# Kernel optimization log

Hardware: AMD Instinct MI355X
Metric: run time of the kernel (lower is better)

## Reference

```python
import jax, jax.numpy as jnp
import numpy as np

NINF = -1000000000.0
B, S, E = 2, 4096, 1024


def setup_inputs() -> dict:
    key = jax.random.key(0)
    ks = jax.random.split(key, 10)
    scale = 1.0 / np.sqrt(E)
    return {
        "query": jax.random.normal(ks[0], (B, S, E), dtype=jnp.float32),
        "key": jax.random.normal(ks[1], (B, S, E), dtype=jnp.float32),
        "value": jax.random.normal(ks[2], (B, S, E), dtype=jnp.float32),
        "mask": jax.random.randint(ks[3], (S, S), 0, 2).astype(bool),
        "Wq": jax.random.normal(ks[4], (E, E), dtype=jnp.float32) * scale,
        "bq": jnp.zeros((E,), dtype=jnp.float32),
        "Wk": jax.random.normal(ks[5], (E, E), dtype=jnp.float32) * scale,
        "bk": jnp.zeros((E,), dtype=jnp.float32),
        "Wv": jax.random.normal(ks[6], (E, E), dtype=jnp.float32) * scale,
        "bv": jnp.zeros((E,), dtype=jnp.float32),
    }


def reference(query, key, value, mask, Wq, bq, Wk, bk, Wv, bv):
    # linear projections (nn.Linear convention: x @ W.T + b)
    q = jnp.einsum('bse,fe->bsf', query, Wq) + bq   # [B,S,E]
    k = jnp.einsum('bse,fe->bsf', key, Wk) + bk
    v = jnp.einsum('bse,fe->bsf', value, Wv) + bv
    # full QK^T score matrix [B,S,S], scaled by sqrt(E) of projected query
    scores = jnp.einsum('bqe,bke->bqk', q, k) / jnp.sqrt(jnp.float32(E))
    scores = jnp.where(mask, jnp.float32(NINF), scores)  # True = ignored
    attn = jax.nn.softmax(scores, axis=-1)
    return jnp.einsum('bqk,bkv->bqv', attn, v)
```

## Files before the change

### kernel.cpp

```cpp
#include <hip/hip_runtime.h>
#include <hip/hip_bf16.h>


typedef _Float16 f16_t;
typedef _Float16 f16x8 __attribute__((ext_vector_type(8)));
typedef float f32x4 __attribute__((ext_vector_type(4)));
typedef unsigned long long u64;
typedef unsigned int uint;

union PackH8 { f16x8 v; f16_t e[8]; };

__device__ __forceinline__ f32x4 mfma_f16(f16x8 a, f16x8 b, f32x4 c) {
  return __builtin_amdgcn_mfma_f32_16x16x32_f16(a, b, c, 0, 0, 0);
}

__device__ __forceinline__ void cp16(const f16_t* g, f16_t* l) {
  __builtin_amdgcn_global_load_lds(
      (const __attribute__((address_space(1))) unsigned int*)g,
      (__attribute__((address_space(3))) unsigned int*)l, 16, 0, 0);
}

__global__ __launch_bounds__(256) void cvt_mask(
    const float* __restrict__ q, const float* __restrict__ k,
    const float* __restrict__ v, const float* __restrict__ wq,
    const float* __restrict__ wk, const float* __restrict__ wv,
    const int* __restrict__ mask,
    f16_t* __restrict__ xq, f16_t* __restrict__ xk, f16_t* __restrict__ xv,
    f16_t* __restrict__ wqh, f16_t* __restrict__ wkh, f16_t* __restrict__ wvh,
    u64* __restrict__ mb) {
  if (blockIdx.y == 6) {
    const int lane = threadIdx.x & 63;
    int wid = blockIdx.x * 4 + (threadIdx.x >> 6);
    for (int w = wid; w < 262144; w += 16384) {
      const int pred = mask[(size_t)w * 64 + lane] != 0;
      u64 b = __ballot(pred);
      if (lane == 0) mb[w] = b;
    }
    return;
  }
  const float* src; f16_t* dst; size_t n;
  switch (blockIdx.y) {
    case 0: src = q;  dst = xq;  n = 8388608; break;
    case 1: src = k;  dst = xk;  n = 8388608; break;
    case 2: src = v;  dst = xv;  n = 8388608; break;
    case 3: src = wq; dst = wqh; n = 1048576; break;
    case 4: src = wk; dst = wkh; n = 1048576; break;
    default: src = wv; dst = wvh; n = 1048576; break;
  }
  size_t i = ((size_t)blockIdx.x * 256 + threadIdx.x) * 8;
  if (i >= n) return;
  float4 a = *(const float4*)(src + i);
  float4 b = *(const float4*)(src + i + 4);
  PackH8 p;
  p.e[0] = (f16_t)a.x; p.e[1] = (f16_t)a.y; p.e[2] = (f16_t)a.z; p.e[3] = (f16_t)a.w;
  p.e[4] = (f16_t)b.x; p.e[5] = (f16_t)b.y; p.e[6] = (f16_t)b.z; p.e[7] = (f16_t)b.w;
  *(f16x8*)(dst + i) = p.v;
}

#define TK 64

__device__ __forceinline__ void core8ph(
    const f16_t* __restrict__ Ab, const f16_t* __restrict__ Bb,
    int m0, int n0, int K, int iters, f32x4 (&acc)[4][8]) {
  __shared__ f16_t lA[32768];
  __shared__ f16_t lB[32768];

  const int tid = threadIdx.x;
  const int w = tid >> 6, lane = tid & 63;
  const int quad = lane >> 4, l15 = lane & 15;
  const int wm = w >> 1, wn = w & 1;
  const int srow = lane >> 2;
  const int sg = (lane & 3) ^ (srow & 3);
  const int Km = K - 1;

  const uint aoff0 = (uint)(m0 + w * 32 + srow) * K + sg * 8;
  const uint aoff1 = aoff0 + 16 * K;
  const uint boff0 = (uint)(n0 + w * 32 + srow) * K + sg * 8;
  const uint boff1 = boff0 + 16 * K;
  const int ld0 = (w * 32) * 32;
  const int ld1 = (w * 32 + 16) * 32;

  int afo[4], bfo[8];
  const int swz = (quad ^ (l15 & 3)) * 8;
#pragma unroll
  for (int mi = 0; mi < 4; mi++) afo[mi] = (wm * 64 + mi * 16 + l15) * 32 + swz;
#pragma unroll
  for (int ni = 0; ni < 8; ni++) bfo[ni] = (wn * 128 + ni * 16 + l15) * 32 + swz;

#define STG_A(sl, kb) { cp16(Ab + aoff0 + (kb), lA + (sl) * 8192 + ld0); \
                        cp16(Ab + aoff1 + (kb), lA + (sl) * 8192 + ld1); }
#define STG_B(sl, kb) { cp16(Bb + boff0 + (kb), lB + (sl) * 8192 + ld0); \
                        cp16(Bb + boff1 + (kb), lB + (sl) * 8192 + ld1); }

  STG_A(0, 0) STG_B(0, 0)
  STG_A(1, 32) STG_B(1, 32)
  STG_A(2, 64) STG_B(2, 64)
  asm volatile("s_waitcnt vmcnt(4)" ::: "memory");
  __builtin_amdgcn_s_barrier();

  f16x8 af[4], bf[8];

#define PH(SL, Q, STG, VMW) { \
    if ((Q) == 0) { \
      _Pragma("unroll") for (int mi = 0; mi < 4; mi++) \
        af[mi] = *(const f16x8*)(lA + (SL) * 8192 + afo[mi]); \
      _Pragma("unroll") for (int ni = 0; ni < 4; ni++) \
        bf[ni] = *(const f16x8*)(lB + (SL) * 8192 + bfo[ni]); \
    } else { \
      _Pragma("unroll") for (int ni = 4; ni < 8; ni++) \
        bf[ni] = *(const f16x8*)(lB + (SL) * 8192 + bfo[ni]); \
    } \
    STG \
    asm volatile("" ::: "memory"); \
    __builtin_amdgcn_s_barrier(); \
    asm volatile("s_waitcnt lgkmcnt(0)" ::: "memory"); \
    __builtin_amdgcn_sched_barrier(0); \
    __builtin_amdgcn_s_setprio(1); \
    _Pragma("unroll") for (int mi = 0; mi < 4; mi++) { \
      _Pragma("unroll") for (int nj = 0; nj < 4; nj++) { \
        const int ni = (Q) * 4 + nj; \
        acc[mi][ni] = mfma_f16(af[mi], bf[ni], acc[mi][ni]); \
      } } \
    __builtin_amdgcn_sched_barrier(0); \
    __builtin_amdgcn_s_setprio(0); \
    VMW \
    asm volatile("" ::: "memory"); \
    __builtin_amdgcn_s_barrier(); \
  }

#define VM4 asm volatile("s_waitcnt vmcnt(4)" ::: "memory");

  for (int i = 0; i < iters; i++) {
    const int t0 = 2 * i;
    const int kb3 = ((t0 + 1) * 64 + 32) & Km;
    const int kb0 = ((t0 + 2) * 64) & Km;
    const int kb1 = kb0 + 32;
    const int kb2 = ((t0 + 3) * 64) & Km;
    PH(0, 0, STG_A(3, kb3), )
    PH(0, 1, STG_B(3, kb3), )
    PH(1, 0, STG_A(0, kb0), )
    PH(1, 1, STG_B(0, kb0), VM4)
    PH(2, 0, STG_A(1, kb1), )
    PH(2, 1, STG_B(1, kb1), )
    PH(3, 0, STG_A(2, kb2), )
    PH(3, 1, STG_B(2, kb2), VM4)
  }

  asm volatile("s_waitcnt vmcnt(0)" ::: "memory");
#undef PH
#undef VM4
#undef STG_A
#undef STG_B
}

__global__ __launch_bounds__(512, 2) void gemm512(
    const f16_t* __restrict__ A, const f16_t* __restrict__ B,
    f16_t* __restrict__ C, const float* __restrict__ bias0,
    const float* __restrict__ bias1, int K,
    long sAz, long sBz, long sCz, float scale0, float scale1, int Cstride) {
  const int bz = blockIdx.z;
  const int n0 = blockIdx.x * 256;
  const int m0 = blockIdx.y * 256;
  const f16_t* Ab = A + (size_t)sAz * bz;
  const f16_t* Bb = B + (size_t)sBz * bz;

  f32x4 acc[4][8] = {};
  core8ph(Ab, Bb, m0, n0, K, K >> 7, acc);

  const int tid = threadIdx.x;
  const int w = tid >> 6, lane = tid & 63;
  const int quad = lane >> 4, l15 = lane & 15;
  const int wm = w >> 1, wn = w & 1;
  const float* bias = bz ? bias1 : bias0;
  const float scale = bz ? scale1 : scale0;
  f16_t* Cb = C + (size_t)sCz * bz;
#pragma unroll
  for (int mi = 0; mi < 4; mi++) {
#pragma unroll
    for (int ni = 0; ni < 8; ni++) {
      const int gm0 = m0 + wm * 64 + mi * 16 + quad * 4;
      const int gn = n0 + wn * 128 + ni * 16 + l15;
#pragma unroll
      for (int r = 0; r < 4; r++) {
        const int gm = gm0 + r;
        Cb[(size_t)gm * Cstride + gn] = (f16_t)((acc[mi][ni][r] + bias[gn]) * scale);
      }
    }
  }
}

__global__ __launch_bounds__(256, 2) void gemm256(
    const f16_t* __restrict__ A, const f16_t* __restrict__ B,
    f16_t* __restrict__ C, const float* __restrict__ bias0, int K) {
  __shared__ f16_t sA[256 * TK];
  __shared__ f16_t sB[128 * TK];

  const int n0 = blockIdx.x * 128;
  const int m0 = blockIdx.y * 256;
  const int tid = threadIdx.x;
  const int w = tid >> 6, lane = tid & 63;
  const int quad = lane >> 4, l15 = lane & 15;
  const int lr = lane >> 3, ls = lane & 7;
  const int sw = ls ^ lr;

  const f16_t* ga[8];
  const f16_t* gb[4];
#pragma unroll
  for (int j = 0; j < 8; j++)
    ga[j] = A + (size_t)(m0 + w * 64 + j * 8 + lr) * K + sw * 8;
#pragma unroll
  for (int j = 0; j < 4; j++)
    gb[j] = B + (size_t)(n0 + w * 32 + j * 8 + lr) * K + sw * 8;

  f32x4 acc[4][8] = {};

  for (int k0 = 0; k0 < K; k0 += TK) {
    __syncthreads();
#pragma unroll
    for (int j = 0; j < 8; j++) cp16(ga[j] + k0, &sA[(w * 64 + j * 8) * TK]);
#pragma unroll
    for (int j = 0; j < 4; j++) cp16(gb[j] + k0, &sB[(w * 32 + j * 8) * TK]);
    __syncthreads();
#pragma unroll
    for (int ks = 0; ks < 2; ks++) {
      f16x8 af[4], bf[8];
#pragma unroll
      for (int mi = 0; mi < 4; mi++) {
        const int row = w * 64 + mi * 16 + l15;
        const int sg = (ks * 4 + quad) ^ (row & 7);
        af[mi] = *(const f16x8*)&sA[row * TK + sg * 8];
      }
#pragma unroll
      for (int ni = 0; ni < 8; ni++) {
        const int row = ni * 16 + l15;
        const int sg = (ks * 4 + quad) ^ (row & 7);
        bf[ni] = *(const f16x8*)&sB[row * TK + sg * 8];
      }
#pragma unroll
      for (int mi = 0; mi < 4; mi++)
#pragma unroll
        for (int ni = 0; ni < 8; ni++)
          acc[mi][ni] = mfma_f16(af[mi], bf[ni], acc[mi][ni]);
    }
  }

#pragma unroll
  for (int mi = 0; mi < 4; mi++) {
#pragma unroll
    for (int ni = 0; ni < 8; ni++) {
      const int gm0 = m0 + w * 64 + mi * 16 + quad * 4;
      const int gn = n0 + ni * 16 + l15;
#pragma unroll
      for (int r = 0; r < 4; r++) {
        const int gm = gm0 + r;
        const int bb = gn >> 12;
        const int s = gn & 4095;
        C[(size_t)bb * 4194304 + (size_t)gm * 4096 + s] =
            (f16_t)(acc[mi][ni][r] + bias0[gm]);
      }
    }
  }
}

__global__ __launch_bounds__(512, 2) void gemm_qk(
    const f16_t* __restrict__ A, const f16_t* __restrict__ B,
    f16_t* __restrict__ S, const u64* __restrict__ mb,
    float* __restrict__ lrow) {
  const int bz = blockIdx.z;
  const int n0 = blockIdx.x * 256;
  const int m0 = blockIdx.y * 256;
  const f16_t* Ab = A + (size_t)4194304 * bz;
  const f16_t* Bb = B + (size_t)4194304 * bz;

  f32x4 acc[4][8] = {};
  core8ph(Ab, Bb, m0, n0, 1024, 8, acc);

  const int tid = threadIdx.x;
  const int w = tid >> 6, lane = tid & 63;
  const int quad = lane >> 4, l15 = lane & 15;
  const int wm = w >> 1, wn = w & 1;
  f16_t* Sb = S + (size_t)16777216 * bz;
  float* lb = lrow + bz * 4096;
  const int wbase = (n0 >> 6) + wn * 2;
#pragma unroll
  for (int mi = 0; mi < 4; mi++) {
#pragma unroll
    for (int r = 0; r < 4; r++) {
      const int gm = m0 + wm * 64 + mi * 16 + quad * 4 + r;
      const u64 w0 = mb[(size_t)gm * 64 + wbase];
      const u64 w1 = mb[(size_t)gm * 64 + wbase + 1];
      float rs = 0.f;
#pragma unroll
      for (int ni = 0; ni < 8; ni++) {
        const int col_l = ni * 16 + l15;
        const u64 mw = (ni < 4) ? w0 : w1;
        const int bit = (int)((mw >> (col_l & 63)) & 1);
        const float p = bit ? 0.f : __expf(acc[mi][ni][r] - 3.0f);
        Sb[(size_t)gm * 4096 + n0 + wn * 128 + col_l] = (f16_t)p;
        rs += p;
      }
      rs += __shfl_xor(rs, 1); rs += __shfl_xor(rs, 2);
      rs += __shfl_xor(rs, 4); rs += __shfl_xor(rs, 8);
      if (l15 == 0) atomicAdd(&lb[gm], rs);
    }
  }
}

__global__ __launch_bounds__(256) void gemm_pv(
    const f16_t* __restrict__ S, const f16_t* __restrict__ V,
    float* __restrict__ O, const float* __restrict__ lrow) {
  __shared__ f16_t sA[128 * TK];
  __shared__ f16_t sB[128 * TK];
  const int bid = blockIdx.x;
  const int bz = bid >> 8;
  const int r8 = bid & 255;
  const int xcd = r8 & 7;
  const int j = r8 >> 3;
  const int m0 = (xcd * 4 + (j >> 3)) * 128;
  const int n0 = (j & 7) * 128;

  const int tid = threadIdx.x;
  const int w = tid >> 6, lane = tid & 63;
  const int quad = lane >> 4, l15 = lane & 15;
  const int wm = w >> 1, wn = w & 1;
  const int lr = lane >> 3, ls = lane & 7;
  const int sw = ls ^ lr;

  const f16_t* Ab = S + (size_t)16777216 * bz;
  const f16_t* Bb = V + (size_t)4194304 * bz;

  const f16_t* ga[4];
  const f16_t* gb[4];
#pragma unroll
  for (int jj = 0; jj < 4; jj++) {
    ga[jj] = Ab + (size_t)(m0 + w * 32 + jj * 8 + lr) * 4096 + sw * 8;
    gb[jj] = Bb + (size_t)(n0 + w * 32 + jj * 8 + lr) * 4096 + sw * 8;
  }

  f32x4 acc[4][4] = {};

  for (int k0 = 0; k0 < 4096; k0 += TK) {
    __syncthreads();
#pragma unroll
    for (int jj = 0; jj < 4; jj++) {
      cp16(ga[jj] + k0, &sA[(w * 32 + jj * 8) * TK]);
      cp16(gb[jj] + k0, &sB[(w * 32 + jj * 8) * TK]);
    }
    __syncthreads();
#pragma unroll
    for (int ks = 0; ks < 2; ks++) {
      f16x8 af[4], bf[4];
#pragma unroll
      for (int mi = 0; mi < 4; mi++) {
        const int row = wm * 64 + mi * 16 + l15;
        const int sg = (ks * 4 + quad) ^ (row & 7);
        af[mi] = *(const f16x8*)&sA[row * TK + sg * 8];
      }
#pragma unroll
      for (int ni = 0; ni < 4; ni++) {
        const int row = wn * 64 + ni * 16 + l15;
        const int sg = (ks * 4 + quad) ^ (row & 7);
        bf[ni] = *(const f16x8*)&sB[row * TK + sg * 8];
      }
#pragma unroll
      for (int mi = 0; mi < 4; mi++)
#pragma unroll
        for (int ni = 0; ni < 4; ni++)
          acc[mi][ni] = mfma_f16(af[mi], bf[ni], acc[mi][ni]);
    }
  }

  float* Ob = O + (size_t)4194304 * bz;
  const float* lb = lrow + bz * 4096;
#pragma unroll
  for (int mi = 0; mi < 4; mi++) {
#pragma unroll
    for (int ni = 0; ni < 4; ni++) {
      const int gm0 = m0 + wm * 64 + mi * 16 + quad * 4;
      const int gn = n0 + wn * 64 + ni * 16 + l15;
#pragma unroll
      for (int r = 0; r < 4; r++) {
        const int gm = gm0 + r;
        Ob[(size_t)gm * 1024 + gn] = acc[mi][ni][r] * (1.0f / lb[gm]);
      }
    }
  }
}

extern "C" void kernel_launch(void* const* d_in, const int* in_sizes, int n_in,
                              void* d_out, int out_size, void* d_ws, size_t ws_size,
                              hipStream_t stream) {
  const float* query = (const float*)d_in[0];
  const float* key_  = (const float*)d_in[1];
  const float* value = (const float*)d_in[2];
  const int* mask    = (const int*)d_in[3];
  const float* Wq = (const float*)d_in[4];
  const float* bq = (const float*)d_in[5];
  const float* Wk = (const float*)d_in[6];
  const float* bk = (const float*)d_in[7];
  const float* Wv = (const float*)d_in[8];
  const float* bv = (const float*)d_in[9];
  float* out = (float*)d_out;

  const size_t MB = (size_t)1 << 20;
  char* w = (char*)d_ws;
  f16_t* qb  = (f16_t*)(w);
  f16_t* kb  = (f16_t*)(w + 16 * MB);
  f16_t* vt  = (f16_t*)(w + 32 * MB);
  f16_t* xq  = (f16_t*)(w + 48 * MB);
  f16_t* xk  = (f16_t*)(w + 64 * MB);
  f16_t* xv  = (f16_t*)(w + 80 * MB);
  f16_t* wqh = (f16_t*)(w + 96 * MB);
  f16_t* wkh = (f16_t*)(w + 98 * MB);
  f16_t* wvh = (f16_t*)(w + 100 * MB);
  f16_t* S   = (f16_t*)(w + 48 * MB);
  float* ls  = (float*)(w + 112 * MB);
  u64* mb = (u64*)d_out;

  cvt_mask<<<dim3(4096, 7), 256, 0, stream>>>(query, key_, value, Wq, Wk, Wv,
                                              mask, xq, xk, xv, wqh, wkh, wvh, mb);
  gemm512<<<dim3(4, 32, 2), 512, 0, stream>>>(
      xq, wqh, qb, bq, bk, 1024, 8388608L, 1048576L, 8388608L,
      0.03125f, 1.0f, 1024);
  gemm256<<<dim3(64, 4), 256, 0, stream>>>(wvh, xv, vt, bv, 1024);
  hipMemsetAsync(ls, 0, 2 * 4096 * sizeof(float), stream);
  gemm_qk<<<dim3(16, 16, 2), 512, 0, stream>>>(qb, kb, S, mb, ls);
  gemm_pv<<<dim3(512), 256, 0, stream>>>(S, vt, out, ls);
}
```

Measured before the change: 433.5 us.

## Port V-projection and PV GEMMs to multi-stage pipelined core, remap QK blocks per XCD

Adds a 4-stage pipelined 256x128 GEMM core (core4ph) with async global-to-LDS loads and phase barriers, and uses it for the V projection and the PV GEMM in place of their single-buffered loops. The PV GEMM moves from 128x128 tiles on 256 threads to 256x128 tiles on 512 threads, and the QK GEMM gets a flat grid with XCD-aware block remapping for L2 locality. The main loop now peels its last iteration, so no wrapped-around prefetches are issued and the K mask is dropped. The LDS swizzle pattern is also changed. This adds complexity and raises LDS use per block.

```diff
diff --git a/kernel.cpp b/kernel.cpp
--- a/kernel.cpp
+++ b/kernel.cpp
@@ -70,8 +70,7 @@
   const int quad = lane >> 4, l15 = lane & 15;
   const int wm = w >> 1, wn = w & 1;
   const int srow = lane >> 2;
-  const int sg = (lane & 3) ^ (srow & 3);
-  const int Km = K - 1;
+  const int sg = (lane & 3) ^ ((lane >> 3) & 3);
 
   const uint aoff0 = (uint)(m0 + w * 32 + srow) * K + sg * 8;
   const uint aoff1 = aoff0 + 16 * K;
@@ -81,7 +80,7 @@
   const int ld1 = (w * 32 + 16) * 32;
 
   int afo[4], bfo[8];
-  const int swz = (quad ^ (l15 & 3)) * 8;
+  const int swz = (quad ^ ((l15 >> 1) & 3)) * 8;
 #pragma unroll
   for (int mi = 0; mi < 4; mi++) afo[mi] = (wm * 64 + mi * 16 + l15) * 32 + swz;
 #pragma unroll
@@ -129,13 +128,14 @@
   }
 
 #define VM4 asm volatile("s_waitcnt vmcnt(4)" ::: "memory");
-
-  for (int i = 0; i < iters; i++) {
+#define VM0 asm volatile("s_waitcnt vmcnt(0)" ::: "memory");
+
+  for (int i = 0; i < iters - 1; i++) {
     const int t0 = 2 * i;
-    const int kb3 = ((t0 + 1) * 64 + 32) & Km;
-    const int kb0 = ((t0 + 2) * 64) & Km;
+    const int kb3 = (t0 + 1) * 64 + 32;
+    const int kb0 = (t0 + 2) * 64;
     const int kb1 = kb0 + 32;
-    const int kb2 = ((t0 + 3) * 64) & Km;
+    const int kb2 = (t0 + 3) * 64;
     PH(0, 0, STG_A(3, kb3), )
     PH(0, 1, STG_B(3, kb3), )
     PH(1, 0, STG_A(0, kb0), )
@@ -145,12 +145,103 @@
     PH(3, 0, STG_A(2, kb2), )
     PH(3, 1, STG_B(2, kb2), VM4)
   }
-
-  asm volatile("s_waitcnt vmcnt(0)" ::: "memory");
+  {
+    const int kbp = K - 32;
+    PH(0, 0, STG_A(3, kbp), )
+    PH(0, 1, STG_B(3, kbp), )
+    PH(1, 0, , )
+    PH(1, 1, , VM0)
+    PH(2, 0, , )
+    PH(2, 1, , )
+    PH(3, 0, , )
+    PH(3, 1, , )
+  }
 #undef PH
-#undef VM4
 #undef STG_A
 #undef STG_B
+}
+
+__device__ __forceinline__ void core4ph(
+    const f16_t* __restrict__ Ab, const f16_t* __restrict__ Bb,
+    int m0, int n0, int K, int iters, f32x4 (&acc)[4][4]) {
+  __shared__ f16_t lA[32768];
+  __shared__ f16_t lB[16384];
+
+  const int tid = threadIdx.x;
+  const int w = tid >> 6, lane = tid & 63;
+  const int quad = lane >> 4, l15 = lane & 15;
+  const int wm = w >> 1, wn = w & 1;
+  const int sg = (lane & 3) ^ ((lane >> 3) & 3);
+
+  const uint arow = (uint)(w * 16 + (lane >> 2));
+  const uint aoff0 = (uint)(m0 + arow) * K + sg * 8;
+  const uint aoff1 = aoff0 + 128 * K;
+  const uint boff  = (uint)(n0 + arow) * K + sg * 8;
+  const int ldw = w * 512;
+
+  int afo[4], bfo[4];
+  const int swz = (quad ^ ((l15 >> 1) & 3)) * 8;
+#pragma unroll
+  for (int mi = 0; mi < 4; mi++) afo[mi] = (wm * 64 + mi * 16 + l15) * 32 + swz;
+#pragma unroll
+  for (int ni = 0; ni < 4; ni++) bfo[ni] = (wn * 64 + ni * 16 + l15) * 32 + swz;
+
+#define STG4(sl, kb) { cp16(Ab + aoff0 + (kb), lA + (sl) * 8192 + ldw); \
+                       cp16(Ab + aoff1 + (kb), lA + (sl) * 8192 + 4096 + ldw); \
+                       cp16(Bb + boff  + (kb), lB + (sl) * 4096 + ldw); }
+
+  STG4(0, 0)
+  STG4(1, 32)
+  STG4(2, 64)
+  asm volatile("s_waitcnt vmcnt(3)" ::: "memory");
+  __builtin_amdgcn_s_barrier();
+
+  f16x8 af[4], bf[4];
+
+#define PH4(SL, STG, VMW) { \
+    _Pragma("unroll") for (int mi = 0; mi < 4; mi++) \
+      af[mi] = *(const f16x8*)(lA + (SL) * 8192 + afo[mi]); \
+    _Pragma("unroll") for (int ni = 0; ni < 4; ni++) \
+      bf[ni] = *(const f16x8*)(lB + (SL) * 4096 + bfo[ni]); \
+    STG \
+    asm volatile("" ::: "memory"); \
+    __builtin_amdgcn_s_barrier(); \
+    asm volatile("s_waitcnt lgkmcnt(0)" ::: "memory"); \
+    __builtin_amdgcn_sched_barrier(0); \
+    __builtin_amdgcn_s_setprio(1); \
+    _Pragma("unroll") for (int mi = 0; mi < 4; mi++) { \
+      _Pragma("unroll") for (int ni = 0; ni < 4; ni++) { \
+        acc[mi][ni] = mfma_f16(af[mi], bf[ni], acc[mi][ni]); \
+      } } \
+    __builtin_amdgcn_sched_barrier(0); \
+    __builtin_amdgcn_s_setprio(0); \
+    VMW \
+    asm volatile("" ::: "memory"); \
+    __builtin_amdgcn_s_barrier(); \
+  }
+
+#define VM6 asm volatile("s_waitcnt vmcnt(6)" ::: "memory");
+#define VM3 asm volatile("s_waitcnt vmcnt(3)" ::: "memory");
+
+  for (int i = 0; i < iters - 1; i++) {
+    const int t0 = 2 * i;
+    PH4(0, STG4(3, (t0 + 1) * 64 + 32), VM6)
+    PH4(1, STG4(0, (t0 + 2) * 64), VM6)
+    PH4(2, STG4(1, (t0 + 2) * 64 + 32), VM6)
+    PH4(3, STG4(2, (t0 + 3) * 64), VM6)
+  }
+  {
+    PH4(0, STG4(3, K - 32), VM6)
+    PH4(1, , VM3)
+    PH4(2, , VM0)
+    PH4(3, , )
+  }
+#undef PH4
+#undef STG4
+#undef VM6
+#undef VM3
+#undef VM4
+#undef VM0
 }
 
 __global__ __launch_bounds__(512, 2) void gemm512(
@@ -189,67 +280,25 @@
   }
 }
 
-__global__ __launch_bounds__(256, 2) void gemm256(
+__global__ __launch_bounds__(512, 2) void gemm256(
     const f16_t* __restrict__ A, const f16_t* __restrict__ B,
     f16_t* __restrict__ C, const float* __restrict__ bias0, int K) {
-  __shared__ f16_t sA[256 * TK];
-  __shared__ f16_t sB[128 * TK];
-
   const int n0 = blockIdx.x * 128;
   const int m0 = blockIdx.y * 256;
-  const int tid = threadIdx.x;
-  const int w = tid >> 6, lane = tid & 63;
-  const int quad = lane >> 4, l15 = lane & 15;
-  const int lr = lane >> 3, ls = lane & 7;
-  const int sw = ls ^ lr;
-
-  const f16_t* ga[8];
-  const f16_t* gb[4];
-#pragma unroll
-  for (int j = 0; j < 8; j++)
-    ga[j] = A + (size_t)(m0 + w * 64 + j * 8 + lr) * K + sw * 8;
-#pragma unroll
-  for (int j = 0; j < 4; j++)
-    gb[j] = B + (size_t)(n0 + w * 32 + j * 8 + lr) * K + sw * 8;
-
-  f32x4 acc[4][8] = {};
-
-  for (int k0 = 0; k0 < K; k0 += TK) {
-    __syncthreads();
-#pragma unroll
-    for (int j = 0; j < 8; j++) cp16(ga[j] + k0, &sA[(w * 64 + j * 8) * TK]);
-#pragma unroll
-    for (int j = 0; j < 4; j++) cp16(gb[j] + k0, &sB[(w * 32 + j * 8) * TK]);
-    __syncthreads();
-#pragma unroll
-    for (int ks = 0; ks < 2; ks++) {
-      f16x8 af[4], bf[8];
-#pragma unroll
-      for (int mi = 0; mi < 4; mi++) {
-        const int row = w * 64 + mi * 16 + l15;
-        const int sg = (ks * 4 + quad) ^ (row & 7);
-        af[mi] = *(const f16x8*)&sA[row * TK + sg * 8];
-      }
-#pragma unroll
-      for (int ni = 0; ni < 8; ni++) {
-        const int row = ni * 16 + l15;
-        const int sg = (ks * 4 + quad) ^ (row & 7);
-        bf[ni] = *(const f16x8*)&sB[row * TK + sg * 8];
-      }
-#pragma unroll
-      for (int mi = 0; mi < 4; mi++)
-#pragma unroll
-        for (int ni = 0; ni < 8; ni++)
-          acc[mi][ni] = mfma_f16(af[mi], bf[ni], acc[mi][ni]);
-    }
-  }
-
+
+  f32x4 acc[4][4] = {};
+  core4ph(A, B, m0, n0, K, K >> 7, acc);
+
+  const int tid = threadIdx.x;
+  const int w = tid >> 6, lane = tid & 63;
+  const int quad = lane >> 4, l15 = lane & 15;
+  const int wm = w >> 1, wn = w & 1;
 #pragma unroll
   for (int mi = 0; mi < 4; mi++) {
 #pragma unroll
-    for (int ni = 0; ni < 8; ni++) {
-      const int gm0 = m0 + w * 64 + mi * 16 + quad * 4;
-      const int gn = n0 + ni * 16 + l15;
+    for (int ni = 0; ni < 4; ni++) {
+      const int gm0 = m0 + wm * 64 + mi * 16 + quad * 4;
+      const int gn = n0 + wn * 64 + ni * 16 + l15;
 #pragma unroll
       for (int r = 0; r < 4; r++) {
         const int gm = gm0 + r;
@@ -266,9 +315,13 @@
     const f16_t* __restrict__ A, const f16_t* __restrict__ B,
     f16_t* __restrict__ S, const u64* __restrict__ mb,
     float* __restrict__ lrow) {
-  const int bz = blockIdx.z;
-  const int n0 = blockIdx.x * 256;
-  const int m0 = blockIdx.y * 256;
+  const int bid = blockIdx.x;
+  const int xcd = bid & 7;
+  const int l = bid >> 3;
+  const int bz = l >> 5;
+  const int r5 = l & 31;
+  const int m0 = (xcd * 2 + (r5 >> 4)) * 256;
+  const int n0 = (r5 & 15) * 256;
   const f16_t* Ab = A + (size_t)4194304 * bz;
   const f16_t* Bb = B + (size_t)4194304 * bz;
 
@@ -306,70 +359,27 @@
   }
 }
 
-__global__ __launch_bounds__(256) void gemm_pv(
+__global__ __launch_bounds__(512, 2) void gemm_pv(
     const f16_t* __restrict__ S, const f16_t* __restrict__ V,
     float* __restrict__ O, const float* __restrict__ lrow) {
-  __shared__ f16_t sA[128 * TK];
-  __shared__ f16_t sB[128 * TK];
   const int bid = blockIdx.x;
-  const int bz = bid >> 8;
-  const int r8 = bid & 255;
-  const int xcd = r8 & 7;
-  const int j = r8 >> 3;
-  const int m0 = (xcd * 4 + (j >> 3)) * 128;
-  const int n0 = (j & 7) * 128;
-
-  const int tid = threadIdx.x;
-  const int w = tid >> 6, lane = tid & 63;
-  const int quad = lane >> 4, l15 = lane & 15;
-  const int wm = w >> 1, wn = w & 1;
-  const int lr = lane >> 3, ls = lane & 7;
-  const int sw = ls ^ lr;
+  const int xcd = bid & 7;
+  const int l = bid >> 3;
+  const int bz = l >> 4;
+  const int r4 = l & 15;
+  const int m0 = (xcd * 2 + (r4 >> 3)) * 256;
+  const int n0 = (r4 & 7) * 128;
 
   const f16_t* Ab = S + (size_t)16777216 * bz;
   const f16_t* Bb = V + (size_t)4194304 * bz;
 
-  const f16_t* ga[4];
-  const f16_t* gb[4];
-#pragma unroll
-  for (int jj = 0; jj < 4; jj++) {
-    ga[jj] = Ab + (size_t)(m0 + w * 32 + jj * 8 + lr) * 4096 + sw * 8;
-    gb[jj] = Bb + (size_t)(n0 + w * 32 + jj * 8 + lr) * 4096 + sw * 8;
-  }
-
   f32x4 acc[4][4] = {};
-
-  for (int k0 = 0; k0 < 4096; k0 += TK) {
-    __syncthreads();
-#pragma unroll
-    for (int jj = 0; jj < 4; jj++) {
-      cp16(ga[jj] + k0, &sA[(w * 32 + jj * 8) * TK]);
-      cp16(gb[jj] + k0, &sB[(w * 32 + jj * 8) * TK]);
-    }
-    __syncthreads();
-#pragma unroll
-    for (int ks = 0; ks < 2; ks++) {
-      f16x8 af[4], bf[4];
-#pragma unroll
-      for (int mi = 0; mi < 4; mi++) {
-        const int row = wm * 64 + mi * 16 + l15;
-        const int sg = (ks * 4 + quad) ^ (row & 7);
-        af[mi] = *(const f16x8*)&sA[row * TK + sg * 8];
-      }
-#pragma unroll
-      for (int ni = 0; ni < 4; ni++) {
-        const int row = wn * 64 + ni * 16 + l15;
-        const int sg = (ks * 4 + quad) ^ (row & 7);
-        bf[ni] = *(const f16x8*)&sB[row * TK + sg * 8];
-      }
-#pragma unroll
-      for (int mi = 0; mi < 4; mi++)
-#pragma unroll
-        for (int ni = 0; ni < 4; ni++)
-          acc[mi][ni] = mfma_f16(af[mi], bf[ni], acc[mi][ni]);
-    }
-  }
-
+  core4ph(Ab, Bb, m0, n0, 4096, 32, acc);
+
+  const int tid = threadIdx.x;
+  const int w = tid >> 6, lane = tid & 63;
+  const int quad = lane >> 4, l15 = lane & 15;
+  const int wm = w >> 1, wn = w & 1;
   float* Ob = O + (size_t)4194304 * bz;
   const float* lb = lrow + bz * 4096;
 #pragma unroll
@@ -422,8 +432,8 @@
   gemm512<<<dim3(4, 32, 2), 512, 0, stream>>>(
       xq, wqh, qb, bq, bk, 1024, 8388608L, 1048576L, 8388608L,
       0.03125f, 1.0f, 1024);
-  gemm256<<<dim3(64, 4), 256, 0, stream>>>(wvh, xv, vt, bv, 1024);
+  gemm256<<<dim3(64, 4), 512, 0, stream>>>(wvh, xv, vt, bv, 1024);
   hipMemsetAsync(ls, 0, 2 * 4096 * sizeof(float), stream);
-  gemm_qk<<<dim3(16, 16, 2), 512, 0, stream>>>(qb, kb, S, mb, ls);
-  gemm_pv<<<dim3(512), 256, 0, stream>>>(S, vt, out, ls);
-}
+  gemm_qk<<<dim3(512), 512, 0, stream>>>(qb, kb, S, mb, ls);
+  gemm_pv<<<dim3(256), 512, 0, stream>>>(S, vt, out, ls);
+}
```

Result: no change. 436.2 us (+0.6%).
